# Kernel tuning notes

Hardware: AMD Instinct MI355X
Metric: run time of the kernel (lower is better)

## Reference

```python
import jax, jax.numpy as jnp
import numpy as np

K_MAX = 32
TEMP = 1.0
EPS = 1e-08


def setup_inputs() -> dict:
    key = jax.random.key(0)
    k1, k2, k3, k4 = jax.random.split(key, 4)
    S, N, d_k, d_A, B = 8, 100000, 64, 2048, 64
    scale = d_A ** (-0.5)
    return {
        "z": jax.random.normal(k1, (B, d_A), dtype=jnp.float32),
        "pool_keys": jax.random.normal(k2, (S, N, d_k), dtype=jnp.float32),
        "W_Q": jax.random.normal(k3, (S, d_k, d_A), dtype=jnp.float32) * scale,
        "aspect_weights": jnp.zeros((S,), dtype=jnp.float32),
        "tau": jnp.zeros((), dtype=jnp.float32),
        "lambda_val": jnp.float32(10.0),
        "is_warmup": 0,
    }


def reference(z, pool_keys, W_Q, aspect_weights, tau, lambda_val, is_warmup):
    # Aspect query projections: [B, S, d_k]
    queries = jnp.einsum('ska,ba->bsk', W_Q, z)
    qn = queries / (jnp.linalg.norm(queries, axis=-1, keepdims=True) + EPS)
    kn = pool_keys / (jnp.linalg.norm(pool_keys, axis=-1, keepdims=True) + EPS)
    # Multi-aspect cosine similarity: [B, S, N]
    sim = jnp.einsum('bsk,snk->bsn', qn, kn)
    w = jax.nn.softmax(aspect_weights, axis=0)          # [S]
    s_i = jnp.einsum('s,bsn->bn', w, sim)               # [B, N]

    if is_warmup:
        scores, idx = jax.lax.top_k(s_i, K_MAX)
        alpha = jax.nn.softmax(scores / TEMP, axis=-1)
        return alpha, idx
    else:
        g = jax.nn.sigmoid(lambda_val * (s_i - tau))
        raw = g * jnp.exp(s_i / TEMP)
        raw = raw / (raw.sum(axis=-1, keepdims=True) + EPS)
        top_raw, idx = jax.lax.top_k(raw, K_MAX)
        alpha = top_raw / (top_raw.sum(axis=-1, keepdims=True) + EPS)
        return alpha, idx
```

## Files before the change

### kernel.cpp

```cpp
#include <hip/hip_runtime.h>
#include <math.h>

#define SA    8
#define NKEYS 100000
#define NP    100096
#define DK    64
#define DA    2048
#define BB    64
#define KMAX  32
static constexpr float EPSF = 1e-8f;

typedef short  bf16x8 __attribute__((ext_vector_type(8)));
typedef float  f32x4  __attribute__((ext_vector_type(4)));

__device__ inline void split2(float x, unsigned short& h, unsigned short& l) {
  unsigned u = __float_as_uint(x);
  unsigned r = u + 0x7FFFu + ((u >> 16) & 1u);
  h = (unsigned short)(r >> 16);
  float hf = __uint_as_float(r & 0xFFFF0000u);
  float lo = x - hf;
  unsigned ul = __float_as_uint(lo);
  unsigned rl = ul + 0x7FFFu + ((ul >> 16) & 1u);
  l = (unsigned short)(rl >> 16);
}

__global__ __launch_bounds__(256) void k_queries(const float* __restrict__ z,
                                                 const float* __restrict__ WQ,
                                                 float* __restrict__ q) {
  const int t = blockIdx.x * 4 + (threadIdx.x >> 6);
  const int lane = threadIdx.x & 63;
  const int b = t >> 9, sk = t & 511;
  const float4* w4 = (const float4*)WQ + (size_t)sk * 512;
  const float4* z4 = (const float4*)z + (size_t)b * 512;
  float acc = 0.f;
#pragma unroll
  for (int i = 0; i < 8; ++i) {
    float4 a = w4[lane + 64 * i];
    float4 c = z4[lane + 64 * i];
    acc = fmaf(a.x, c.x, fmaf(a.y, c.y, fmaf(a.z, c.z, fmaf(a.w, c.w, acc))));
  }
#pragma unroll
  for (int o = 32; o; o >>= 1) acc += __shfl_xor(acc, o);
  if (lane == 0) q[(b * SA + (sk >> 6)) * DK + (sk & 63)] = acc;
}

__global__ __launch_bounds__(256) void k_norm(const float* __restrict__ q,
                                              const float* __restrict__ aw,
                                              unsigned short* __restrict__ qh,
                                              unsigned short* __restrict__ ql,
                                              float* __restrict__ wbuf) {
  const int t = blockIdx.x * 4 + (threadIdx.x >> 6);
  const int lane = threadIdx.x & 63;
  float x = q[t * DK + lane];
  float ss = x * x;
#pragma unroll
  for (int o = 32; o; o >>= 1) ss += __shfl_xor(ss, o);
  float xn = x / (sqrtf(ss) + EPSF);
  unsigned short h, l;
  split2(xn, h, l);
  const int b = t >> 3, s = t & 7;
  const int o = (s * BB + b) * DK + lane;
  qh[o] = h; ql[o] = l;
  if (blockIdx.x == 0 && threadIdx.x == 0) {
    float m = -INFINITY;
    for (int s2 = 0; s2 < SA; ++s2) m = fmaxf(m, aw[s2]);
    float e[SA], sum = 0.f;
    for (int s2 = 0; s2 < SA; ++s2) { e[s2] = __expf(aw[s2] - m); sum += e[s2]; }
    for (int s2 = 0; s2 < SA; ++s2) wbuf[s2] = e[s2] / sum;
  }
}

__global__ __launch_bounds__(256, 3) void k_sim(const float* __restrict__ pk,
                                                const unsigned short* __restrict__ qh,
                                                const unsigned short* __restrict__ ql,
                                                const float* __restrict__ wbuf,
                                                float* __restrict__ si) {
  __shared__ unsigned short Ah[64 * 64], Al[64 * 64];
  __shared__ unsigned short Bh[128 * 64], Bl[128 * 64];
  const int tid = threadIdx.x;
  const int wave = tid >> 6, lane = tid & 63;
  const int n0 = blockIdx.x * 128;
  const int c16 = tid & 15;
  const int rg  = tid >> 4;
  const int lm = lane & 15, lq = lane >> 4;
  const int wn0 = wave * 32;

  f32x4 acc[4][2];
#pragma unroll
  for (int mi = 0; mi < 4; ++mi)
#pragma unroll
    for (int ni = 0; ni < 2; ++ni) acc[mi][ni] = (f32x4){0.f, 0.f, 0.f, 0.f};

  float4 breg[8];
  auto issueB = [&](int s) {
#pragma unroll
    for (int p = 0; p < 8; ++p) {
      int n = n0 + rg + 16 * p; if (n >= NKEYS) n = NKEYS - 1;
      breg[p] = *(const float4*)(pk + ((size_t)s * NKEYS + n) * DK + c16 * 4);
    }
  };
  issueB(0);

  for (int s = 0; s < SA; ++s) {
    ushort4 arh[4], arl[4];
#pragma unroll
    for (int p = 0; p < 4; ++p) {
      int r = rg + 16 * p;
      int o = (s * BB + r) * DK + c16 * 4;
      arh[p] = *(const ushort4*)(qh + o);
      arl[p] = *(const ushort4*)(ql + o);
    }
    const float wsc = wbuf[s];
    float ssr[8];
#pragma unroll
    for (int p = 0; p < 8; ++p) {
      float4 v = breg[p];
      float d = v.x * v.x + v.y * v.y + v.z * v.z + v.w * v.w;
      d += __shfl_xor(d, 1); d += __shfl_xor(d, 2);
      d += __shfl_xor(d, 4); d += __shfl_xor(d, 8);
      ssr[p] = d;
    }
#pragma unroll
    for (int p = 0; p < 8; ++p) {
      int r = rg + 16 * p;
      float sc = wsc / (sqrtf(ssr[p]) + EPSF);
      float4 v = breg[p];
      v.x *= sc; v.y *= sc; v.z *= sc; v.w *= sc;
      ushort4 hv, lv;
      split2(v.x, hv.x, lv.x); split2(v.y, hv.y, lv.y);
      split2(v.z, hv.z, lv.z); split2(v.w, hv.w, lv.w);
      int widx = r * 64 + (((c16 >> 1) ^ (r & 7)) << 3) + ((c16 & 1) << 2);
      *(ushort4*)(Bh + widx) = hv;
      *(ushort4*)(Bl + widx) = lv;
    }
#pragma unroll
    for (int p = 0; p < 4; ++p) {
      int r = rg + 16 * p;
      int widx = r * 64 + (((c16 >> 1) ^ (r & 7)) << 3) + ((c16 & 1) << 2);
      *(ushort4*)(Ah + widx) = arh[p];
      *(ushort4*)(Al + widx) = arl[p];
    }
    __syncthreads();
    if (s < SA - 1) issueB(s + 1);
#pragma unroll
    for (int kk = 0; kk < 2; ++kk) {
      const int chp = (((kk * 4 + lq) ^ (lm & 7)) << 3);
      bf16x8 ah[4], al2[4], bh2[2], bl2[2];
#pragma unroll
      for (int mi = 0; mi < 4; ++mi) {
        int off = (mi * 16 + lm) * 64 + chp;
        ah[mi]  = *(const bf16x8*)(Ah + off);
        al2[mi] = *(const bf16x8*)(Al + off);
      }
#pragma unroll
      for (int ni = 0; ni < 2; ++ni) {
        int off = (wn0 + ni * 16 + lm) * 64 + chp;
        bh2[ni] = *(const bf16x8*)(Bh + off);
        bl2[ni] = *(const bf16x8*)(Bl + off);
      }
#pragma unroll
      for (int mi = 0; mi < 4; ++mi)
#pragma unroll
        for (int ni = 0; ni < 2; ++ni) {
          acc[mi][ni] = __builtin_amdgcn_mfma_f32_16x16x32_bf16(ah[mi],  bh2[ni], acc[mi][ni], 0, 0, 0);
          acc[mi][ni] = __builtin_amdgcn_mfma_f32_16x16x32_bf16(ah[mi],  bl2[ni], acc[mi][ni], 0, 0, 0);
          acc[mi][ni] = __builtin_amdgcn_mfma_f32_16x16x32_bf16(al2[mi], bh2[ni], acc[mi][ni], 0, 0, 0);
          acc[mi][ni] = __builtin_amdgcn_mfma_f32_16x16x32_bf16(al2[mi], bl2[ni], acc[mi][ni], 0, 0, 0);
        }
    }
    __syncthreads();
  }
#pragma unroll
  for (int mi = 0; mi < 4; ++mi)
#pragma unroll
    for (int ni = 0; ni < 2; ++ni) {
      int n = n0 + wn0 + ni * 16 + lm;
      if (n < NKEYS) {
#pragma unroll
        for (int r = 0; r < 4; ++r) {
          int m = mi * 16 + lq * 4 + r;
          si[(size_t)m * NP + n] = acc[mi][ni][r];
        }
      }
    }
}

__global__ __launch_bounds__(256) void k_topk_a(const float* __restrict__ si,
                                                const float* __restrict__ lam_p,
                                                const float* __restrict__ tau_p,
                                                float* __restrict__ candv,
                                                int* __restrict__ candi,
                                                float* __restrict__ Rp) {
  const int b = blockIdx.x >> 3, sl = blockIdx.x & 7;
  const int tid = threadIdx.x, wave = tid >> 6, lane = tid & 63;
  const float lam = lam_p[0], tau = tau_p[0];
  const float* row = si + (size_t)b * NP;

  float cv = -INFINITY; int ci = 0;
  float r = 0.f;
  float thr = -INFINITY;

  int c = sl + 8 * wave;
  float4 f0 = *(const float4*)(row + c * 256 + lane * 4);
  int cn = (c + 32 < 391) ? c + 32 : c;
  float4 f1 = *(const float4*)(row + cn * 256 + lane * 4);
  while (c < 391) {
    const int n0 = c * 256;
    float4 v4 = f0;
    f0 = f1;
    int cp = (c + 64 < 391) ? c + 64 : c;
    f1 = *(const float4*)(row + cp * 256 + lane * 4);
    c += 32;
#pragma unroll
    for (int e = 0; e < 4; ++e) {
      float x = (e == 0) ? v4.x : (e == 1) ? v4.y : (e == 2) ? v4.z : v4.w;
      int n = n0 + lane * 4 + e;
      bool valid = n < NKEYS;
      if (valid) {
        float g = 1.f / (1.f + __expf(-lam * (x - tau)));
        r += g * __expf(x);
      }
      unsigned long long m = __ballot(valid && (x > thr));
      while (m) {
        int src = __ffsll((unsigned long long)m) - 1;
        m &= m - 1;
        float xv = __shfl(x, src);
        int xi = n0 + src * 4 + e;
        bool bigger = (cv > xv) || (cv == xv && ci < xi);
        unsigned long long bm = __ballot(bigger);
        int pos = __popcll(bm);
        float sv = __shfl_up(cv, 1);
        int sidx = __shfl_up(ci, 1);
        if (lane == pos)      { cv = xv; ci = xi; }
        else if (lane > pos)  { cv = sv; ci = sidx; }
        thr = __shfl(cv, 31);
      }
    }
  }
#pragma unroll
  for (int o = 32; o; o >>= 1) r += __shfl_xor(r, o);

  __shared__ float lv[4][64];
  __shared__ int   li[4][64];
  __shared__ float lr[4];
  lv[wave][lane] = cv; li[wave][lane] = ci;
  if (lane == 0) lr[wave] = r;
  __syncthreads();

  if (wave == 0) {
    float R = lr[0] + lr[1] + lr[2] + lr[3];
    for (int w = 1; w < 4; ++w) {
      float nv = lv[w][lane]; int ni = li[w][lane];
      float rv = __shfl_xor(nv, 63); int ri = __shfl_xor(ni, 63);
      bool take = (rv > cv) || (rv == cv && ri < ci);
      if (take) { cv = rv; ci = ri; }
#pragma unroll
      for (int j = 32; j; j >>= 1) {
        float ov = __shfl_xor(cv, j); int oi = __shfl_xor(ci, j);
        bool lower = (lane & j) == 0;
        bool ob = (ov > cv) || (ov == cv && oi < ci);
        if (ob == lower) { cv = ov; ci = oi; }
      }
    }
    if (lane < KMAX) {
      candv[(b * 8 + sl) * KMAX + lane] = cv;
      candi[(b * 8 + sl) * KMAX + lane] = ci;
    }
    if (lane == 0) Rp[b * 8 + sl] = R;
  }
}

__global__ __launch_bounds__(64) void k_topk_b(const float* __restrict__ candv,
                                               const int* __restrict__ candi,
                                               const float* __restrict__ Rp,
                                               const float* __restrict__ lam_p,
                                               const float* __restrict__ tau_p,
                                               const int* __restrict__ warm_p,
                                               float* __restrict__ out) {
  const int b = blockIdx.x, lane = threadIdx.x;
  const float lam = lam_p[0], tau = tau_p[0];
  const int warm = warm_p[0];

  float R = 0.f;
#pragma unroll
  for (int sl = 0; sl < 8; ++sl) R += Rp[b * 8 + sl];

  float cv = (lane < KMAX) ? candv[b * 8 * KMAX + lane] : -INFINITY;
  int   ci = (lane < KMAX) ? candi[b * 8 * KMAX + lane] : 0x7FFFFFFF;
  for (int sl = 1; sl < 8; ++sl) {
    float nv = (lane < KMAX) ? candv[(b * 8 + sl) * KMAX + lane] : -INFINITY;
    int   ni = (lane < KMAX) ? candi[(b * 8 + sl) * KMAX + lane] : 0x7FFFFFFF;
    float rv = __shfl_xor(nv, 63); int ri = __shfl_xor(ni, 63);
    bool take = (rv > cv) || (rv == cv && ri < ci);
    if (take) { cv = rv; ci = ri; }
#pragma unroll
    for (int j = 32; j; j >>= 1) {
      float ov = __shfl_xor(cv, j); int oi = __shfl_xor(ci, j);
      bool lower = (lane & j) == 0;
      bool ob = (ov > cv) || (ov == cv && oi < ci);
      if (ob == lower) { cv = ov; ci = oi; }
    }
  }
  float t = 0.f;
  if (warm) {
    float mm = __shfl(cv, 0);
    if (lane < KMAX) t = __expf(cv - mm);
    float ssum = t;
#pragma unroll
    for (int o = 32; o; o >>= 1) ssum += __shfl_xor(ssum, o);
    if (lane < KMAX) {
      out[b * KMAX + lane] = t / ssum;
      out[BB * KMAX + b * KMAX + lane] = (float)ci;
    }
  } else {
    if (lane < KMAX) {
      float g = 1.f / (1.f + __expf(-lam * (cv - tau)));
      t = g * __expf(cv) / (R + EPSF);
    }
    float ssum = t;
#pragma unroll
    for (int o = 32; o; o >>= 1) ssum += __shfl_xor(ssum, o);
    if (lane < KMAX) {
      out[b * KMAX + lane] = t / (ssum + EPSF);
      out[BB * KMAX + b * KMAX + lane] = (float)ci;
    }
  }
}

extern "C" void kernel_launch(void* const* d_in, const int* in_sizes, int n_in,
                              void* d_out, int out_size, void* d_ws, size_t ws_size,
                              hipStream_t stream) {
  const float* z   = (const float*)d_in[0];
  const float* pk  = (const float*)d_in[1];
  const float* WQ  = (const float*)d_in[2];
  const float* aw  = (const float*)d_in[3];
  const float* tau = (const float*)d_in[4];
  const float* lam = (const float*)d_in[5];
  const int* warm  = (const int*)d_in[6];
  float* out = (float*)d_out;

  float* w = (float*)d_ws;
  float* q     = w;
  float* wbuf  = w + 32768;
  float* Rp    = w + 32832;
  float* candv = w + 33344;
  int*   candi = (int*)(w + 49728);
  unsigned short* qh = (unsigned short*)(w + 66112);
  unsigned short* ql = (unsigned short*)(w + 82496);
  float* si    = w + 98880;

  k_queries<<<dim3(8192), 256, 0, stream>>>(z, WQ, q);
  k_norm<<<dim3(128), 256, 0, stream>>>(q, aw, qh, ql, wbuf);
  k_sim<<<dim3((NKEYS + 127) / 128), 256, 0, stream>>>(pk, qh, ql, wbuf, si);
  k_topk_a<<<dim3(512), 256, 0, stream>>>(si, lam, tau, candv, candi, Rp);
  k_topk_b<<<dim3(BB), 64, 0, stream>>>(candv, candi, Rp, lam, tau, warm, out);
}
```

Baseline: 372.1 us.

## Register-tile query projection and fuse two-stage top-k into one kernel

k_queries now has each wave compute a 4x4 tile of (batch, sk) dot products, so every loaded W_Q and z vector is reused four times, and the grid shrinks from 8192 to 512 blocks. The two top-k kernels are merged into one with a single 512-thread block per row, which removes the candidate buffers and one launch. It also adds an early skip inside the ballot loop when a candidate falls below the current threshold. The trade-off is that top-k now runs on only 64 blocks with 8 waves each and prefetches one chunk ahead instead of two, so the row scan may have less parallelism and less latency hiding.

```diff
diff --git a/kernel.cpp b/kernel.cpp
--- a/kernel.cpp
+++ b/kernel.cpp
@@ -27,21 +27,45 @@
 __global__ __launch_bounds__(256) void k_queries(const float* __restrict__ z,
                                                  const float* __restrict__ WQ,
                                                  float* __restrict__ q) {
-  const int t = blockIdx.x * 4 + (threadIdx.x >> 6);
+  const int wid = blockIdx.x * 4 + (threadIdx.x >> 6);
   const int lane = threadIdx.x & 63;
-  const int b = t >> 9, sk = t & 511;
-  const float4* w4 = (const float4*)WQ + (size_t)sk * 512;
-  const float4* z4 = (const float4*)z + (size_t)b * 512;
-  float acc = 0.f;
+  const int b0  = (wid >> 7) * 4;
+  const int sk0 = (wid & 127) * 4;
+  const float4* w4 = (const float4*)WQ;
+  const float4* z4 = (const float4*)z;
+  float acc[4][4];
+#pragma unroll
+  for (int bi = 0; bi < 4; ++bi)
+#pragma unroll
+    for (int j = 0; j < 4; ++j) acc[bi][j] = 0.f;
 #pragma unroll
   for (int i = 0; i < 8; ++i) {
-    float4 a = w4[lane + 64 * i];
-    float4 c = z4[lane + 64 * i];
-    acc = fmaf(a.x, c.x, fmaf(a.y, c.y, fmaf(a.z, c.z, fmaf(a.w, c.w, acc))));
-  }
-#pragma unroll
-  for (int o = 32; o; o >>= 1) acc += __shfl_xor(acc, o);
-  if (lane == 0) q[(b * SA + (sk >> 6)) * DK + (sk & 63)] = acc;
+    float4 wr[4], zr[4];
+#pragma unroll
+    for (int j = 0; j < 4; ++j)  wr[j]  = w4[(size_t)(sk0 + j) * 512 + lane + 64 * i];
+#pragma unroll
+    for (int bi = 0; bi < 4; ++bi) zr[bi] = z4[(size_t)(b0 + bi) * 512 + lane + 64 * i];
+#pragma unroll
+    for (int bi = 0; bi < 4; ++bi)
+#pragma unroll
+      for (int j = 0; j < 4; ++j) {
+        acc[bi][j] = fmaf(wr[j].x, zr[bi].x, acc[bi][j]);
+        acc[bi][j] = fmaf(wr[j].y, zr[bi].y, acc[bi][j]);
+        acc[bi][j] = fmaf(wr[j].z, zr[bi].z, acc[bi][j]);
+        acc[bi][j] = fmaf(wr[j].w, zr[bi].w, acc[bi][j]);
+      }
+  }
+#pragma unroll
+  for (int bi = 0; bi < 4; ++bi)
+#pragma unroll
+    for (int j = 0; j < 4; ++j) {
+#pragma unroll
+      for (int o = 32; o; o >>= 1) acc[bi][j] += __shfl_xor(acc[bi][j], o);
+    }
+  if (lane < 16) {
+    const int bi = lane >> 2, j = lane & 3;
+    q[(size_t)(b0 + bi) * 512 + sk0 + j] = acc[bi][j];
+  }
 }
 
 __global__ __launch_bounds__(256) void k_norm(const float* __restrict__ q,
@@ -185,13 +209,12 @@
     }
 }
 
-__global__ __launch_bounds__(256) void k_topk_a(const float* __restrict__ si,
-                                                const float* __restrict__ lam_p,
-                                                const float* __restrict__ tau_p,
-                                                float* __restrict__ candv,
-                                                int* __restrict__ candi,
-                                                float* __restrict__ Rp) {
-  const int b = blockIdx.x >> 3, sl = blockIdx.x & 7;
+__global__ __launch_bounds__(512) void k_topk(const float* __restrict__ si,
+                                              const float* __restrict__ lam_p,
+                                              const float* __restrict__ tau_p,
+                                              const int* __restrict__ warm_p,
+                                              float* __restrict__ out) {
+  const int b = blockIdx.x;
   const int tid = threadIdx.x, wave = tid >> 6, lane = tid & 63;
   const float lam = lam_p[0], tau = tau_p[0];
   const float* row = si + (size_t)b * NP;
@@ -200,17 +223,13 @@
   float r = 0.f;
   float thr = -INFINITY;
 
-  int c = sl + 8 * wave;
+  int c = wave;
   float4 f0 = *(const float4*)(row + c * 256 + lane * 4);
-  int cn = (c + 32 < 391) ? c + 32 : c;
-  float4 f1 = *(const float4*)(row + cn * 256 + lane * 4);
   while (c < 391) {
     const int n0 = c * 256;
+    const int cn = (c + 8 < 391) ? c + 8 : c;
     float4 v4 = f0;
-    f0 = f1;
-    int cp = (c + 64 < 391) ? c + 64 : c;
-    f1 = *(const float4*)(row + cp * 256 + lane * 4);
-    c += 32;
+    f0 = *(const float4*)(row + cn * 256 + lane * 4);
 #pragma unroll
     for (int e = 0; e < 4; ++e) {
       float x = (e == 0) ? v4.x : (e == 1) ? v4.y : (e == 2) ? v4.z : v4.w;
@@ -225,6 +244,7 @@
         int src = __ffsll((unsigned long long)m) - 1;
         m &= m - 1;
         float xv = __shfl(x, src);
+        if (xv < thr) continue;
         int xi = n0 + src * 4 + e;
         bool bigger = (cv > xv) || (cv == xv && ci < xi);
         unsigned long long bm = __ballot(bigger);
@@ -236,20 +256,23 @@
         thr = __shfl(cv, 31);
       }
     }
+    c += 8;
   }
 #pragma unroll
   for (int o = 32; o; o >>= 1) r += __shfl_xor(r, o);
 
-  __shared__ float lv[4][64];
-  __shared__ int   li[4][64];
-  __shared__ float lr[4];
+  __shared__ float lv[8][64];
+  __shared__ int   li[8][64];
+  __shared__ float lr[8];
   lv[wave][lane] = cv; li[wave][lane] = ci;
   if (lane == 0) lr[wave] = r;
   __syncthreads();
 
   if (wave == 0) {
-    float R = lr[0] + lr[1] + lr[2] + lr[3];
-    for (int w = 1; w < 4; ++w) {
+    float R = 0.f;
+#pragma unroll
+    for (int w = 0; w < 8; ++w) R += lr[w];
+    for (int w = 1; w < 8; ++w) {
       float nv = lv[w][lane]; int ni = li[w][lane];
       float rv = __shfl_xor(nv, 63); int ri = __shfl_xor(ni, 63);
       bool take = (rv > cv) || (rv == cv && ri < ci);
@@ -262,67 +285,30 @@
         if (ob == lower) { cv = ov; ci = oi; }
       }
     }
-    if (lane < KMAX) {
-      candv[(b * 8 + sl) * KMAX + lane] = cv;
-      candi[(b * 8 + sl) * KMAX + lane] = ci;
-    }
-    if (lane == 0) Rp[b * 8 + sl] = R;
-  }
-}
-
-__global__ __launch_bounds__(64) void k_topk_b(const float* __restrict__ candv,
-                                               const int* __restrict__ candi,
-                                               const float* __restrict__ Rp,
-                                               const float* __restrict__ lam_p,
-                                               const float* __restrict__ tau_p,
-                                               const int* __restrict__ warm_p,
-                                               float* __restrict__ out) {
-  const int b = blockIdx.x, lane = threadIdx.x;
-  const float lam = lam_p[0], tau = tau_p[0];
-  const int warm = warm_p[0];
-
-  float R = 0.f;
-#pragma unroll
-  for (int sl = 0; sl < 8; ++sl) R += Rp[b * 8 + sl];
-
-  float cv = (lane < KMAX) ? candv[b * 8 * KMAX + lane] : -INFINITY;
-  int   ci = (lane < KMAX) ? candi[b * 8 * KMAX + lane] : 0x7FFFFFFF;
-  for (int sl = 1; sl < 8; ++sl) {
-    float nv = (lane < KMAX) ? candv[(b * 8 + sl) * KMAX + lane] : -INFINITY;
-    int   ni = (lane < KMAX) ? candi[(b * 8 + sl) * KMAX + lane] : 0x7FFFFFFF;
-    float rv = __shfl_xor(nv, 63); int ri = __shfl_xor(ni, 63);
-    bool take = (rv > cv) || (rv == cv && ri < ci);
-    if (take) { cv = rv; ci = ri; }
-#pragma unroll
-    for (int j = 32; j; j >>= 1) {
-      float ov = __shfl_xor(cv, j); int oi = __shfl_xor(ci, j);
-      bool lower = (lane & j) == 0;
-      bool ob = (ov > cv) || (ov == cv && oi < ci);
-      if (ob == lower) { cv = ov; ci = oi; }
-    }
-  }
-  float t = 0.f;
-  if (warm) {
-    float mm = __shfl(cv, 0);
-    if (lane < KMAX) t = __expf(cv - mm);
-    float ssum = t;
-#pragma unroll
-    for (int o = 32; o; o >>= 1) ssum += __shfl_xor(ssum, o);
-    if (lane < KMAX) {
-      out[b * KMAX + lane] = t / ssum;
-      out[BB * KMAX + b * KMAX + lane] = (float)ci;
-    }
-  } else {
-    if (lane < KMAX) {
-      float g = 1.f / (1.f + __expf(-lam * (cv - tau)));
-      t = g * __expf(cv) / (R + EPSF);
-    }
-    float ssum = t;
-#pragma unroll
-    for (int o = 32; o; o >>= 1) ssum += __shfl_xor(ssum, o);
-    if (lane < KMAX) {
-      out[b * KMAX + lane] = t / (ssum + EPSF);
-      out[BB * KMAX + b * KMAX + lane] = (float)ci;
+    const int warm = warm_p[0];
+    float t = 0.f;
+    if (warm) {
+      float mm = __shfl(cv, 0);
+      if (lane < KMAX) t = __expf(cv - mm);
+      float ssum = t;
+#pragma unroll
+      for (int o = 32; o; o >>= 1) ssum += __shfl_xor(ssum, o);
+      if (lane < KMAX) {
+        out[b * KMAX + lane] = t / ssum;
+        out[BB * KMAX + b * KMAX + lane] = (float)ci;
+      }
+    } else {
+      if (lane < KMAX) {
+        float g = 1.f / (1.f + __expf(-lam * (cv - tau)));
+        t = g * __expf(cv) / (R + EPSF);
+      }
+      float ssum = t;
+#pragma unroll
+      for (int o = 32; o; o >>= 1) ssum += __shfl_xor(ssum, o);
+      if (lane < KMAX) {
+        out[b * KMAX + lane] = t / (ssum + EPSF);
+        out[BB * KMAX + b * KMAX + lane] = (float)ci;
+      }
     }
   }
 }
@@ -342,16 +328,12 @@
   float* w = (float*)d_ws;
   float* q     = w;
   float* wbuf  = w + 32768;
-  float* Rp    = w + 32832;
-  float* candv = w + 33344;
-  int*   candi = (int*)(w + 49728);
   unsigned short* qh = (unsigned short*)(w + 66112);
   unsigned short* ql = (unsigned short*)(w + 82496);
   float* si    = w + 98880;
 
-  k_queries<<<dim3(8192), 256, 0, stream>>>(z, WQ, q);
+  k_queries<<<dim3(512), 256, 0, stream>>>(z, WQ, q);
   k_norm<<<dim3(128), 256, 0, stream>>>(q, aw, qh, ql, wbuf);
   k_sim<<<dim3((NKEYS + 127) / 128), 256, 0, stream>>>(pk, qh, ql, wbuf, si);
-  k_topk_a<<<dim3(512), 256, 0, stream>>>(si, lam, tau, candv, candi, Rp);
-  k_topk_b<<<dim3(BB), 64, 0, stream>>>(candv, candi, Rp, lam, tau, warm, out);
-}
+  k_topk<<<dim3(BB), 512, 0, stream>>>(si, lam, tau, warm, out);
+}
```

Result: slower. 411.6 us (+10.6%).
